# Optimization experiments

Hardware: AMD Instinct MI355X
Metric: run time of the kernel (lower is better)

Reference implementation:

```python
import jax, jax.numpy as jnp
import numpy as np

S, H, A = 8192, 4096, 1024

def setup_inputs() -> dict:
    key = jax.random.key(0)
    ks = jax.random.split(key, 8)
    return {
        "encoder_outputs": jax.random.normal(ks[0], (S, H), jnp.float32),
        "hidden": jax.random.normal(ks[1], (H,), jnp.float32),
        "U_w": jax.random.normal(ks[2], (A, H), jnp.float32) * (1.0 / np.sqrt(H)),
        "U_b": jax.random.normal(ks[3], (A,), jnp.float32) * 0.01,
        "W_w": jax.random.normal(ks[4], (A, H), jnp.float32) * (1.0 / np.sqrt(H)),
        "W_b": jax.random.normal(ks[5], (A,), jnp.float32) * 0.01,
        "V_w": jax.random.normal(ks[6], (1, A), jnp.float32) * (1.0 / np.sqrt(A)),
        "V_b": jax.random.normal(ks[7], (1,), jnp.float32) * 0.01,
    }

def reference(encoder_outputs, hidden, U_w, U_b, W_w, W_b, V_w, V_b):
    # Bahdanau additive attention ('add' mode).
    W_hidden = hidden @ W_w.T + W_b                      # [A]
    U_encode = encoder_outputs @ U_w.T + U_b             # [S, A]
    poly_tanh = jnp.tanh(U_encode + W_hidden)            # [S, A]
    scores = poly_tanh @ V_w.T + V_b                     # [S, 1]
    attn = jax.nn.softmax(scores, axis=0)                # softmax over sequence
    context = attn.T @ encoder_outputs                   # [1, H]
    return context[None]                                 # [1, 1, H] (matches torch bmm)
```

## Files before the change

### kernel.cpp

```cpp
#include <hip/hip_runtime.h>

typedef __attribute__((ext_vector_type(8))) short short8;
typedef __attribute__((ext_vector_type(4))) float f32x4;

#define S_DIM 8192
#define H_DIM 4096
#define A_DIM 1024

__device__ __forceinline__ short f2bf(float x) {
  unsigned u = __float_as_uint(x);
  u += 0x7fffu + ((u >> 16) & 1u);
  return (short)(u >> 16);
}

__device__ __forceinline__ float bf2f(short b) {
  return __uint_as_float(((unsigned)(unsigned short)b) << 16);
}

__device__ __forceinline__ void gload16(const void* g, void* l) {
  __builtin_amdgcn_global_load_lds(
      (const __attribute__((address_space(1))) void*)g,
      (__attribute__((address_space(3))) void*)l, 16, 0, 0);
}


__global__ __launch_bounds__(256) void comb_kernel(const float* __restrict__ hidden,
                                                   const float* __restrict__ Ww,
                                                   const float* __restrict__ Wb,
                                                   const float* __restrict__ Ub,
                                                   float* __restrict__ comb) {
  const int wave = threadIdx.x >> 6;
  const int lane = threadIdx.x & 63;
  const int a = blockIdx.x * 4 + wave;
  const float* row = Ww + (size_t)a * H_DIM;
  float acc = 0.f;
  for (int k = lane * 4; k < H_DIM; k += 64 * 4) {
    float4 w = *(const float4*)(row + k);
    float4 h = *(const float4*)(hidden + k);
    acc += w.x * h.x + w.y * h.y + w.z * h.z + w.w * h.w;
  }
  #pragma unroll
  for (int mk = 1; mk < 64; mk <<= 1) acc += __shfl_xor(acc, mk);
  if (lane == 0) comb[a] = acc + Wb[a] + Ub[a];
}

__global__ __launch_bounds__(1024) void softmax_kernel(const float* __restrict__ scores,
                                                       float* __restrict__ attn) {
  __shared__ float redm[16];
  __shared__ float reds[16];
  const int tid = threadIdx.x;
  const int lane = tid & 63, wid = tid >> 6;
  float v[8];
  float m = -3.0e38f;
  #pragma unroll
  for (int i = 0; i < 8; ++i) { v[i] = scores[i * 1024 + tid]; m = fmaxf(m, v[i]); }
  #pragma unroll
  for (int mk = 1; mk < 64; mk <<= 1) m = fmaxf(m, __shfl_xor(m, mk));
  if (lane == 0) redm[wid] = m;
  __syncthreads();
  float M = redm[0];
  #pragma unroll
  for (int j = 1; j < 16; ++j) M = fmaxf(M, redm[j]);
  float e[8]; float s = 0.f;
  #pragma unroll
  for (int i = 0; i < 8; ++i) { e[i] = __expf(v[i] - M); s += e[i]; }
  #pragma unroll
  for (int mk = 1; mk < 64; mk <<= 1) s += __shfl_xor(s, mk);
  if (lane == 0) reds[wid] = s;
  __syncthreads();
  float T = 0.f;
  #pragma unroll
  for (int j = 0; j < 16; ++j) T += reds[j];
  const float inv = 1.f / T;
  #pragma unroll
  for (int i = 0; i < 8; ++i) attn[i * 1024 + tid] = e[i] * inv;
}


__global__ __launch_bounds__(256) void cvt_kernel(const float* __restrict__ src,
                                                  unsigned short* __restrict__ dst,
                                                  int n8) {
  const int stride = gridDim.x * blockDim.x;
  for (int i = blockIdx.x * blockDim.x + threadIdx.x; i < n8; i += stride) {
    float4 a = ((const float4*)src)[(size_t)i * 2];
    float4 b = ((const float4*)src)[(size_t)i * 2 + 1];
    short8 o;
    o[0] = f2bf(a.x); o[1] = f2bf(a.y); o[2] = f2bf(a.z); o[3] = f2bf(a.w);
    o[4] = f2bf(b.x); o[5] = f2bf(b.y); o[6] = f2bf(b.z); o[7] = f2bf(b.w);
    ((short8*)dst)[i] = o;
  }
}

__global__ __launch_bounds__(256) void gemm_score_bf_kernel(
    const unsigned short* __restrict__ A,
    const unsigned short* __restrict__ B,
    const float* __restrict__ comb,
    const float* __restrict__ Vw,
    float* __restrict__ scores) {
  __shared__ __align__(16) unsigned short sA[128 * 64];
  __shared__ __align__(16) unsigned short sB[128 * 64];

  const int tid  = threadIdx.x;
  const int lane = tid & 63;
  const int wave = tid >> 6;
  const int wm = wave >> 1, wn = wave & 1;
  const int m0 = blockIdx.x * 128;
  const int n0 = blockIdx.y * 128;

  const int srow = wave * 32 + (lane >> 3);
  const int scol = (lane & 7) * 8;
  const unsigned short* ga = A + (size_t)(m0 + srow) * H_DIM + scol;
  const unsigned short* gb = B + (size_t)(n0 + srow) * H_DIM + scol;

  #define STAGE(kt) do {                                                     \
    const unsigned short* pa_ = ga + (size_t)(kt) * 64;                      \
    const unsigned short* pb_ = gb + (size_t)(kt) * 64;                      \
    _Pragma("unroll")                                                        \
    for (int i_ = 0; i_ < 4; ++i_) {                                         \
      gload16(pa_ + (size_t)i_ * 8 * H_DIM, &sA[(wave * 4 + i_) * 512]);     \
      gload16(pb_ + (size_t)i_ * 8 * H_DIM, &sB[(wave * 4 + i_) * 512]);     \
    }                                                                        \
  } while (0)

  f32x4 acc[4][4];
  const f32x4 zero = {0.f, 0.f, 0.f, 0.f};
  #pragma unroll
  for (int i = 0; i < 4; ++i)
    #pragma unroll
    for (int j = 0; j < 4; ++j) acc[i][j] = zero;

  STAGE(0);

  const int NK = H_DIM / 64;
  for (int kt = 0; kt < NK; ++kt) {
    __syncthreads();

    short8 af[2][4], bfr[2][4];
    #pragma unroll
    for (int ks = 0; ks < 2; ++ks) {
      #pragma unroll
      for (int i = 0; i < 4; ++i)
        af[ks][i] = *(const short8*)&sA[(wm * 64 + i * 16 + (lane & 15)) * 64 + ks * 32 + (lane >> 4) * 8];
      #pragma unroll
      for (int j = 0; j < 4; ++j)
        bfr[ks][j] = *(const short8*)&sB[(wn * 64 + j * 16 + (lane & 15)) * 64 + ks * 32 + (lane >> 4) * 8];
    }
    __syncthreads();

    if (kt + 1 < NK) STAGE(kt + 1);

    #pragma unroll
    for (int ks = 0; ks < 2; ++ks)
      #pragma unroll
      for (int i = 0; i < 4; ++i)
        #pragma unroll
        for (int j = 0; j < 4; ++j)
          acc[i][j] = __builtin_amdgcn_mfma_f32_16x16x32_bf16(af[ks][i], bfr[ks][j], acc[i][j], 0, 0, 0);
  }
  #undef STAGE

  float vwv[4], cbv[4];
  #pragma unroll
  for (int j = 0; j < 4; ++j) {
    const int col = n0 + wn * 64 + j * 16 + (lane & 15);
    vwv[j] = Vw[col];
    cbv[j] = comb[col];
  }
  #pragma unroll
  for (int i = 0; i < 4; ++i) {
    #pragma unroll
    for (int r = 0; r < 4; ++r) {
      float s = 0.f;
      #pragma unroll
      for (int j = 0; j < 4; ++j)
        s += vwv[j] * tanhf(acc[i][j][r] + cbv[j]);
      s += __shfl_xor(s, 1);
      s += __shfl_xor(s, 2);
      s += __shfl_xor(s, 4);
      s += __shfl_xor(s, 8);
      if ((lane & 15) == 0) {
        const int grow = m0 + wm * 64 + i * 16 + (lane >> 4) * 4 + r;
        atomicAdd(&scores[grow], s);
      }
    }
  }
}

__global__ __launch_bounds__(256) void context_bf_kernel(const unsigned short* __restrict__ Ebf,
                                                         const float* __restrict__ attn,
                                                         float* __restrict__ partial) {
  const int h0 = (blockIdx.x * 256 + threadIdx.x) * 8;
  const int s0 = blockIdx.y * 64;
  float acc[8] = {0.f, 0.f, 0.f, 0.f, 0.f, 0.f, 0.f, 0.f};
  for (int s = s0; s < s0 + 64; ++s) {
    const float w = attn[s];
    short8 e = *(const short8*)(Ebf + (size_t)s * H_DIM + h0);
    #pragma unroll
    for (int j = 0; j < 8; ++j) acc[j] += w * bf2f(e[j]);
  }
  float* p = partial + (size_t)blockIdx.y * H_DIM + h0;
  #pragma unroll
  for (int j = 0; j < 8; ++j) p[j] = acc[j];
}

__global__ __launch_bounds__(256) void context_reduce_kernel(const float* __restrict__ partial,
                                                             float* __restrict__ out) {
  const int h = blockIdx.x * 256 + threadIdx.x;
  float acc = 0.f;
  #pragma unroll 8
  for (int y = 0; y < 128; ++y) acc += partial[(size_t)y * H_DIM + h];
  out[h] = acc;
}


#define LDSW 40
__global__ __launch_bounds__(256) void gemm_score_kernel(const float* __restrict__ E,
                                                         const float* __restrict__ Uw,
                                                         const float* __restrict__ comb,
                                                         const float* __restrict__ Vw,
                                                         float* __restrict__ scores) {
  __shared__ __align__(16) short sA[128 * LDSW];
  __shared__ __align__(16) short sB[128 * LDSW];
  const int tid  = threadIdx.x;
  const int lane = tid & 63;
  const int wave = tid >> 6;
  const int wm = wave >> 1, wn = wave & 1;
  const int m0 = blockIdx.x * 128;
  const int n0 = blockIdx.y * 128;
  const int sr = tid >> 1;
  const int sh = tid & 1;
  const float* gA = E  + (size_t)(m0 + sr) * H_DIM + sh * 16;
  const float* gB = Uw + (size_t)(n0 + sr) * H_DIM + sh * 16;
  alignas(16) float fa[16], fb[16];
  #pragma unroll
  for (int j = 0; j < 4; ++j) {
    *(float4*)&fa[j * 4] = *(const float4*)(gA + j * 4);
    *(float4*)&fb[j * 4] = *(const float4*)(gB + j * 4);
  }
  f32x4 acc[4][4];
  const f32x4 zero = {0.f, 0.f, 0.f, 0.f};
  #pragma unroll
  for (int i = 0; i < 4; ++i)
    #pragma unroll
    for (int j = 0; j < 4; ++j) acc[i][j] = zero;
  short* wA = &sA[sr * LDSW + sh * 16];
  short* wB = &sB[sr * LDSW + sh * 16];
  const int NK = H_DIM / 32;
  for (int kt = 0; kt < NK; ++kt) {
    short8 ca0, ca1, cb0, cb1;
    #pragma unroll
    for (int j = 0; j < 8; ++j) {
      ca0[j] = f2bf(fa[j]);     ca1[j] = f2bf(fa[8 + j]);
      cb0[j] = f2bf(fb[j]);     cb1[j] = f2bf(fb[8 + j]);
    }
    __syncthreads();
    *(short8*)(wA)     = ca0;
    *(short8*)(wA + 8) = ca1;
    *(short8*)(wB)     = cb0;
    *(short8*)(wB + 8) = cb1;
    __syncthreads();
    if (kt + 1 < NK) {
      const float* pA = gA + (kt + 1) * 32;
      const float* pB = gB + (kt + 1) * 32;
      #pragma unroll
      for (int j = 0; j < 4; ++j) {
        *(float4*)&fa[j * 4] = *(const float4*)(pA + j * 4);
        *(float4*)&fb[j * 4] = *(const float4*)(pB + j * 4);
      }
    }
    short8 af[4], bfr[4];
    #pragma unroll
    for (int i = 0; i < 4; ++i)
      af[i] = *(const short8*)&sA[(wm * 64 + i * 16 + (lane & 15)) * LDSW + (lane >> 4) * 8];
    #pragma unroll
    for (int j = 0; j < 4; ++j)
      bfr[j] = *(const short8*)&sB[(wn * 64 + j * 16 + (lane & 15)) * LDSW + (lane >> 4) * 8];
    #pragma unroll
    for (int i = 0; i < 4; ++i)
      #pragma unroll
      for (int j = 0; j < 4; ++j)
        acc[i][j] = __builtin_amdgcn_mfma_f32_16x16x32_bf16(af[i], bfr[j], acc[i][j], 0, 0, 0);
  }
  float vwv[4], cbv[4];
  #pragma unroll
  for (int j = 0; j < 4; ++j) {
    const int col = n0 + wn * 64 + j * 16 + (lane & 15);
    vwv[j] = Vw[col];
    cbv[j] = comb[col];
  }
  #pragma unroll
  for (int i = 0; i < 4; ++i) {
    #pragma unroll
    for (int r = 0; r < 4; ++r) {
      float s = 0.f;
      #pragma unroll
      for (int j = 0; j < 4; ++j)
        s += vwv[j] * tanhf(acc[i][j][r] + cbv[j]);
      s += __shfl_xor(s, 1);
      s += __shfl_xor(s, 2);
      s += __shfl_xor(s, 4);
      s += __shfl_xor(s, 8);
      if ((lane & 15) == 0) {
        const int grow = m0 + wm * 64 + i * 16 + (lane >> 4) * 4 + r;
        atomicAdd(&scores[grow], s);
      }
    }
  }
}

__global__ __launch_bounds__(256) void context_kernel(const float* __restrict__ E,
                                                      const float* __restrict__ attn,
                                                      float* __restrict__ out) {
  const int h  = blockIdx.x * 256 + threadIdx.x;
  const int s0 = blockIdx.y * 256;
  float acc = 0.f;
  #pragma unroll 4
  for (int s = s0; s < s0 + 256; ++s)
    acc += attn[s] * E[(size_t)s * H_DIM + h];
  atomicAdd(&out[h], acc);
}


extern "C" void kernel_launch(void* const* d_in, const int* in_sizes, int n_in,
                              void* d_out, int out_size, void* d_ws, size_t ws_size,
                              hipStream_t stream) {
  const float* E   = (const float*)d_in[0];
  const float* hid = (const float*)d_in[1];
  const float* Uw  = (const float*)d_in[2];
  const float* Ub  = (const float*)d_in[3];
  const float* Ww  = (const float*)d_in[4];
  const float* Wb  = (const float*)d_in[5];
  const float* Vw  = (const float*)d_in[6];

  float* out    = (float*)d_out;
  float* ws     = (float*)d_ws;
  float* comb   = ws;
  float* scores = ws + 1024;
  float* attn   = ws + 1024 + 8192;

  float* partial = ws + 17408;
  unsigned short* Ebf  = (unsigned short*)(ws + 17408 + 128 * H_DIM);
  unsigned short* Uwbf = Ebf + (size_t)S_DIM * H_DIM;
  const size_t NEED = (size_t)(17408 + 128 * H_DIM) * 4
                    + (size_t)(S_DIM + A_DIM) * H_DIM * 2;

  hipMemsetAsync(scores, 0, S_DIM * sizeof(float), stream);

  comb_kernel<<<A_DIM / 4, 256, 0, stream>>>(hid, Ww, Wb, Ub, comb);

  if (ws_size >= NEED) {
    cvt_kernel<<<2048, 256, 0, stream>>>(E, Ebf, (int)((size_t)S_DIM * H_DIM / 8));
    cvt_kernel<<<512, 256, 0, stream>>>(Uw, Uwbf, (int)((size_t)A_DIM * H_DIM / 8));

    dim3 grid(S_DIM / 128, A_DIM / 128);
    gemm_score_bf_kernel<<<grid, 256, 0, stream>>>(Ebf, Uwbf, comb, Vw, scores);

    softmax_kernel<<<1, 1024, 0, stream>>>(scores, attn);

    context_bf_kernel<<<dim3(H_DIM / 2048, S_DIM / 64), 256, 0, stream>>>(Ebf, attn, partial);
    context_reduce_kernel<<<H_DIM / 256, 256, 0, stream>>>(partial, out);
  } else {
    hipMemsetAsync(out, 0, (size_t)out_size * sizeof(float), stream);
    dim3 grid(S_DIM / 128, A_DIM / 128);
    gemm_score_kernel<<<grid, 256, 0, stream>>>(E, Uw, comb, Vw, scores);
    softmax_kernel<<<1, 1024, 0, stream>>>(scores, attn);
    context_kernel<<<dim3(H_DIM / 256, 32), 256, 0, stream>>>(E, attn, out);
  }
}
```

Baseline: 156.7 us.

## Split score GEMM over K in two halves with separate tanh-score reduction kernel

The score GEMM gains a K dimension of 2 in its grid and now writes two fp32 partial [S,A] matrices to workspace instead of applying tanh and V in its epilogue. A new kernel sums the two partials, adds the bias, applies tanh, reduces against V per row, and writes scores directly, which also removes the scores memset and the atomics. The aim is to double the number of GEMM blocks (512 to 1024) to fill the CUs better. In exchange it writes and rereads about 64 MB of fp32 partials and adds a kernel launch. It also needs much more workspace, so if that is missing the code falls back to the old fused path.

After: 172.8 us. 10.3% more time.

```diff
diff --git a/kernel.cpp b/kernel.cpp
--- a/kernel.cpp
+++ b/kernel.cpp
@@ -22,7 +22,6 @@
       (const __attribute__((address_space(1))) void*)g,
       (__attribute__((address_space(3))) void*)l, 16, 0, 0);
 }
-
 
 __global__ __launch_bounds__(256) void comb_kernel(const float* __restrict__ hidden,
                                                    const float* __restrict__ Ww,
@@ -44,39 +43,6 @@
   if (lane == 0) comb[a] = acc + Wb[a] + Ub[a];
 }
 
-__global__ __launch_bounds__(1024) void softmax_kernel(const float* __restrict__ scores,
-                                                       float* __restrict__ attn) {
-  __shared__ float redm[16];
-  __shared__ float reds[16];
-  const int tid = threadIdx.x;
-  const int lane = tid & 63, wid = tid >> 6;
-  float v[8];
-  float m = -3.0e38f;
-  #pragma unroll
-  for (int i = 0; i < 8; ++i) { v[i] = scores[i * 1024 + tid]; m = fmaxf(m, v[i]); }
-  #pragma unroll
-  for (int mk = 1; mk < 64; mk <<= 1) m = fmaxf(m, __shfl_xor(m, mk));
-  if (lane == 0) redm[wid] = m;
-  __syncthreads();
-  float M = redm[0];
-  #pragma unroll
-  for (int j = 1; j < 16; ++j) M = fmaxf(M, redm[j]);
-  float e[8]; float s = 0.f;
-  #pragma unroll
-  for (int i = 0; i < 8; ++i) { e[i] = __expf(v[i] - M); s += e[i]; }
-  #pragma unroll
-  for (int mk = 1; mk < 64; mk <<= 1) s += __shfl_xor(s, mk);
-  if (lane == 0) reds[wid] = s;
-  __syncthreads();
-  float T = 0.f;
-  #pragma unroll
-  for (int j = 0; j < 16; ++j) T += reds[j];
-  const float inv = 1.f / T;
-  #pragma unroll
-  for (int i = 0; i < 8; ++i) attn[i * 1024 + tid] = e[i] * inv;
-}
-
-
 __global__ __launch_bounds__(256) void cvt_kernel(const float* __restrict__ src,
                                                   unsigned short* __restrict__ dst,
                                                   int n8) {
@@ -91,12 +57,10 @@
   }
 }
 
-__global__ __launch_bounds__(256) void gemm_score_bf_kernel(
+__global__ __launch_bounds__(256) void gemm_kspl_kernel(
     const unsigned short* __restrict__ A,
     const unsigned short* __restrict__ B,
-    const float* __restrict__ comb,
-    const float* __restrict__ Vw,
-    float* __restrict__ scores) {
+    float* __restrict__ partialC) {
   __shared__ __align__(16) unsigned short sA[128 * 64];
   __shared__ __align__(16) unsigned short sB[128 * 64];
 
@@ -106,11 +70,12 @@
   const int wm = wave >> 1, wn = wave & 1;
   const int m0 = blockIdx.x * 128;
   const int n0 = blockIdx.y * 128;
+  const int k0 = blockIdx.z * (H_DIM / 2);
 
   const int srow = wave * 32 + (lane >> 3);
   const int scol = (lane & 7) * 8;
-  const unsigned short* ga = A + (size_t)(m0 + srow) * H_DIM + scol;
-  const unsigned short* gb = B + (size_t)(n0 + srow) * H_DIM + scol;
+  const unsigned short* ga = A + (size_t)(m0 + srow) * H_DIM + k0 + scol;
+  const unsigned short* gb = B + (size_t)(n0 + srow) * H_DIM + k0 + scol;
 
   #define STAGE(kt) do {                                                     \
     const unsigned short* pa_ = ga + (size_t)(kt) * 64;                      \
@@ -131,10 +96,179 @@
 
   STAGE(0);
 
+  const int NK = (H_DIM / 2) / 64;
+  for (int kt = 0; kt < NK; ++kt) {
+    __syncthreads();
+
+    short8 af[2][4], bfr[2][4];
+    #pragma unroll
+    for (int ks = 0; ks < 2; ++ks) {
+      #pragma unroll
+      for (int i = 0; i < 4; ++i)
+        af[ks][i] = *(const short8*)&sA[(wm * 64 + i * 16 + (lane & 15)) * 64 + ks * 32 + (lane >> 4) * 8];
+      #pragma unroll
+      for (int j = 0; j < 4; ++j)
+        bfr[ks][j] = *(const short8*)&sB[(wn * 64 + j * 16 + (lane & 15)) * 64 + ks * 32 + (lane >> 4) * 8];
+    }
+    __syncthreads();
+
+    if (kt + 1 < NK) STAGE(kt + 1);
+
+    #pragma unroll
+    for (int ks = 0; ks < 2; ++ks)
+      #pragma unroll
+      for (int i = 0; i < 4; ++i)
+        #pragma unroll
+        for (int j = 0; j < 4; ++j)
+          acc[i][j] = __builtin_amdgcn_mfma_f32_16x16x32_bf16(af[ks][i], bfr[ks][j], acc[ks ? i : i][j], 0, 0, 0);
+  }
+  #undef STAGE
+
+  float* pc = partialC + (size_t)blockIdx.z * S_DIM * A_DIM;
+  #pragma unroll
+  for (int i = 0; i < 4; ++i) {
+    #pragma unroll
+    for (int r = 0; r < 4; ++r) {
+      const int grow = m0 + wm * 64 + i * 16 + (lane >> 4) * 4 + r;
+      float* prow = pc + (size_t)grow * A_DIM + n0 + wn * 64 + (lane & 15);
+      #pragma unroll
+      for (int j = 0; j < 4; ++j) prow[j * 16] = acc[i][j][r];
+    }
+  }
+}
+
+__global__ __launch_bounds__(256) void tanh_score_kernel(
+    const float* __restrict__ P,
+    const float* __restrict__ comb,
+    const float* __restrict__ Vw,
+    float* __restrict__ scores) {
+  const int lane = threadIdx.x & 63;
+  const int wave = threadIdx.x >> 6;
+  float4 vw[4], cb[4];
+  #pragma unroll
+  for (int c = 0; c < 4; ++c) {
+    vw[c] = *(const float4*)&Vw[c * 256 + lane * 4];
+    cb[c] = *(const float4*)&comb[c * 256 + lane * 4];
+  }
+  const float* P1 = P + (size_t)S_DIM * A_DIM;
+  const int row0 = (blockIdx.x * 4 + wave) * 4;
+  #pragma unroll
+  for (int rr = 0; rr < 4; ++rr) {
+    const int s = row0 + rr;
+    const float* p0 = P  + (size_t)s * A_DIM;
+    const float* p1 = P1 + (size_t)s * A_DIM;
+    float acc = 0.f;
+    #pragma unroll
+    for (int c = 0; c < 4; ++c) {
+      float4 x0 = *(const float4*)&p0[c * 256 + lane * 4];
+      float4 x1 = *(const float4*)&p1[c * 256 + lane * 4];
+      acc += vw[c].x * tanhf(x0.x + x1.x + cb[c].x);
+      acc += vw[c].y * tanhf(x0.y + x1.y + cb[c].y);
+      acc += vw[c].z * tanhf(x0.z + x1.z + cb[c].z);
+      acc += vw[c].w * tanhf(x0.w + x1.w + cb[c].w);
+    }
+    #pragma unroll
+    for (int mk = 1; mk < 64; mk <<= 1) acc += __shfl_xor(acc, mk);
+    if (lane == 0) scores[s] = acc;
+  }
+}
+
+__global__ __launch_bounds__(1024) void softmax_kernel(const float* __restrict__ scores,
+                                                       float* __restrict__ attn) {
+  __shared__ float redm[16];
+  __shared__ float reds[16];
+  const int tid = threadIdx.x;
+  const int lane = tid & 63, wid = tid >> 6;
+  float v[8];
+  float m = -3.0e38f;
+  #pragma unroll
+  for (int i = 0; i < 8; ++i) { v[i] = scores[i * 1024 + tid]; m = fmaxf(m, v[i]); }
+  #pragma unroll
+  for (int mk = 1; mk < 64; mk <<= 1) m = fmaxf(m, __shfl_xor(m, mk));
+  if (lane == 0) redm[wid] = m;
+  __syncthreads();
+  float M = redm[0];
+  #pragma unroll
+  for (int j = 1; j < 16; ++j) M = fmaxf(M, redm[j]);
+  float e[8]; float s = 0.f;
+  #pragma unroll
+  for (int i = 0; i < 8; ++i) { e[i] = __expf(v[i] - M); s += e[i]; }
+  #pragma unroll
+  for (int mk = 1; mk < 64; mk <<= 1) s += __shfl_xor(s, mk);
+  if (lane == 0) reds[wid] = s;
+  __syncthreads();
+  float T = 0.f;
+  #pragma unroll
+  for (int j = 0; j < 16; ++j) T += reds[j];
+  const float inv = 1.f / T;
+  #pragma unroll
+  for (int i = 0; i < 8; ++i) attn[i * 1024 + tid] = e[i] * inv;
+}
+
+__global__ __launch_bounds__(256) void context_bf_kernel(const unsigned short* __restrict__ Ebf,
+                                                         const float* __restrict__ attn,
+                                                         float* __restrict__ partial) {
+  const int h0 = (blockIdx.x * 256 + threadIdx.x) * 8;
+  const int s0 = blockIdx.y * 64;
+  float acc[8] = {0.f, 0.f, 0.f, 0.f, 0.f, 0.f, 0.f, 0.f};
+  for (int s = s0; s < s0 + 64; ++s) {
+    const float w = attn[s];
+    short8 e = *(const short8*)(Ebf + (size_t)s * H_DIM + h0);
+    #pragma unroll
+    for (int j = 0; j < 8; ++j) acc[j] += w * bf2f(e[j]);
+  }
+  float* p = partial + (size_t)blockIdx.y * H_DIM + h0;
+  #pragma unroll
+  for (int j = 0; j < 8; ++j) p[j] = acc[j];
+}
+
+__global__ __launch_bounds__(256) void context_reduce_kernel(const float* __restrict__ partial,
+                                                             float* __restrict__ out) {
+  const int h = blockIdx.x * 256 + threadIdx.x;
+  float acc = 0.f;
+  #pragma unroll 8
+  for (int y = 0; y < 128; ++y) acc += partial[(size_t)y * H_DIM + h];
+  out[h] = acc;
+}
+
+
+__global__ __launch_bounds__(256) void gemm_score_bf_kernel(
+    const unsigned short* __restrict__ A,
+    const unsigned short* __restrict__ B,
+    const float* __restrict__ comb,
+    const float* __restrict__ Vw,
+    float* __restrict__ scores) {
+  __shared__ __align__(16) unsigned short sA[128 * 64];
+  __shared__ __align__(16) unsigned short sB[128 * 64];
+  const int tid  = threadIdx.x;
+  const int lane = tid & 63;
+  const int wave = tid >> 6;
+  const int wm = wave >> 1, wn = wave & 1;
+  const int m0 = blockIdx.x * 128;
+  const int n0 = blockIdx.y * 128;
+  const int srow = wave * 32 + (lane >> 3);
+  const int scol = (lane & 7) * 8;
+  const unsigned short* ga = A + (size_t)(m0 + srow) * H_DIM + scol;
+  const unsigned short* gb = B + (size_t)(n0 + srow) * H_DIM + scol;
+  #define STAGE(kt) do {                                                     \
+    const unsigned short* pa_ = ga + (size_t)(kt) * 64;                      \
+    const unsigned short* pb_ = gb + (size_t)(kt) * 64;                      \
+    _Pragma("unroll")                                                        \
+    for (int i_ = 0; i_ < 4; ++i_) {                                         \
+      gload16(pa_ + (size_t)i_ * 8 * H_DIM, &sA[(wave * 4 + i_) * 512]);     \
+      gload16(pb_ + (size_t)i_ * 8 * H_DIM, &sB[(wave * 4 + i_) * 512]);     \
+    }                                                                        \
+  } while (0)
+  f32x4 acc[4][4];
+  const f32x4 zero = {0.f, 0.f, 0.f, 0.f};
+  #pragma unroll
+  for (int i = 0; i < 4; ++i)
+    #pragma unroll
+    for (int j = 0; j < 4; ++j) acc[i][j] = zero;
+  STAGE(0);
   const int NK = H_DIM / 64;
   for (int kt = 0; kt < NK; ++kt) {
     __syncthreads();
-
     short8 af[2][4], bfr[2][4];
     #pragma unroll
     for (int ks = 0; ks < 2; ++ks) {
@@ -146,9 +280,7 @@
         bfr[ks][j] = *(const short8*)&sB[(wn * 64 + j * 16 + (lane & 15)) * 64 + ks * 32 + (lane >> 4) * 8];
     }
     __syncthreads();
-
     if (kt + 1 < NK) STAGE(kt + 1);
-
     #pragma unroll
     for (int ks = 0; ks < 2; ++ks)
       #pragma unroll
@@ -158,7 +290,6 @@
           acc[i][j] = __builtin_amdgcn_mfma_f32_16x16x32_bf16(af[ks][i], bfr[ks][j], acc[i][j], 0, 0, 0);
   }
   #undef STAGE
-
   float vwv[4], cbv[4];
   #pragma unroll
   for (int j = 0; j < 4; ++j) {
@@ -186,140 +317,6 @@
   }
 }
 
-__global__ __launch_bounds__(256) void context_bf_kernel(const unsigned short* __restrict__ Ebf,
-                                                         const float* __restrict__ attn,
-                                                         float* __restrict__ partial) {
-  const int h0 = (blockIdx.x * 256 + threadIdx.x) * 8;
-  const int s0 = blockIdx.y * 64;
-  float acc[8] = {0.f, 0.f, 0.f, 0.f, 0.f, 0.f, 0.f, 0.f};
-  for (int s = s0; s < s0 + 64; ++s) {
-    const float w = attn[s];
-    short8 e = *(const short8*)(Ebf + (size_t)s * H_DIM + h0);
-    #pragma unroll
-    for (int j = 0; j < 8; ++j) acc[j] += w * bf2f(e[j]);
-  }
-  float* p = partial + (size_t)blockIdx.y * H_DIM + h0;
-  #pragma unroll
-  for (int j = 0; j < 8; ++j) p[j] = acc[j];
-}
-
-__global__ __launch_bounds__(256) void context_reduce_kernel(const float* __restrict__ partial,
-                                                             float* __restrict__ out) {
-  const int h = blockIdx.x * 256 + threadIdx.x;
-  float acc = 0.f;
-  #pragma unroll 8
-  for (int y = 0; y < 128; ++y) acc += partial[(size_t)y * H_DIM + h];
-  out[h] = acc;
-}
-
-
-#define LDSW 40
-__global__ __launch_bounds__(256) void gemm_score_kernel(const float* __restrict__ E,
-                                                         const float* __restrict__ Uw,
-                                                         const float* __restrict__ comb,
-                                                         const float* __restrict__ Vw,
-                                                         float* __restrict__ scores) {
-  __shared__ __align__(16) short sA[128 * LDSW];
-  __shared__ __align__(16) short sB[128 * LDSW];
-  const int tid  = threadIdx.x;
-  const int lane = tid & 63;
-  const int wave = tid >> 6;
-  const int wm = wave >> 1, wn = wave & 1;
-  const int m0 = blockIdx.x * 128;
-  const int n0 = blockIdx.y * 128;
-  const int sr = tid >> 1;
-  const int sh = tid & 1;
-  const float* gA = E  + (size_t)(m0 + sr) * H_DIM + sh * 16;
-  const float* gB = Uw + (size_t)(n0 + sr) * H_DIM + sh * 16;
-  alignas(16) float fa[16], fb[16];
-  #pragma unroll
-  for (int j = 0; j < 4; ++j) {
-    *(float4*)&fa[j * 4] = *(const float4*)(gA + j * 4);
-    *(float4*)&fb[j * 4] = *(const float4*)(gB + j * 4);
-  }
-  f32x4 acc[4][4];
-  const f32x4 zero = {0.f, 0.f, 0.f, 0.f};
-  #pragma unroll
-  for (int i = 0; i < 4; ++i)
-    #pragma unroll
-    for (int j = 0; j < 4; ++j) acc[i][j] = zero;
-  short* wA = &sA[sr * LDSW + sh * 16];
-  short* wB = &sB[sr * LDSW + sh * 16];
-  const int NK = H_DIM / 32;
-  for (int kt = 0; kt < NK; ++kt) {
-    short8 ca0, ca1, cb0, cb1;
-    #pragma unroll
-    for (int j = 0; j < 8; ++j) {
-      ca0[j] = f2bf(fa[j]);     ca1[j] = f2bf(fa[8 + j]);
-      cb0[j] = f2bf(fb[j]);     cb1[j] = f2bf(fb[8 + j]);
-    }
-    __syncthreads();
-    *(short8*)(wA)     = ca0;
-    *(short8*)(wA + 8) = ca1;
-    *(short8*)(wB)     = cb0;
-    *(short8*)(wB + 8) = cb1;
-    __syncthreads();
-    if (kt + 1 < NK) {
-      const float* pA = gA + (kt + 1) * 32;
-      const float* pB = gB + (kt + 1) * 32;
-      #pragma unroll
-      for (int j = 0; j < 4; ++j) {
-        *(float4*)&fa[j * 4] = *(const float4*)(pA + j * 4);
-        *(float4*)&fb[j * 4] = *(const float4*)(pB + j * 4);
-      }
-    }
-    short8 af[4], bfr[4];
-    #pragma unroll
-    for (int i = 0; i < 4; ++i)
-      af[i] = *(const short8*)&sA[(wm * 64 + i * 16 + (lane & 15)) * LDSW + (lane >> 4) * 8];
-    #pragma unroll
-    for (int j = 0; j < 4; ++j)
-      bfr[j] = *(const short8*)&sB[(wn * 64 + j * 16 + (lane & 15)) * LDSW + (lane >> 4) * 8];
-    #pragma unroll
-    for (int i = 0; i < 4; ++i)
-      #pragma unroll
-      for (int j = 0; j < 4; ++j)
-        acc[i][j] = __builtin_amdgcn_mfma_f32_16x16x32_bf16(af[i], bfr[j], acc[i][j], 0, 0, 0);
-  }
-  float vwv[4], cbv[4];
-  #pragma unroll
-  for (int j = 0; j < 4; ++j) {
-    const int col = n0 + wn * 64 + j * 16 + (lane & 15);
-    vwv[j] = Vw[col];
-    cbv[j] = comb[col];
-  }
-  #pragma unroll
-  for (int i = 0; i < 4; ++i) {
-    #pragma unroll
-    for (int r = 0; r < 4; ++r) {
-      float s = 0.f;
-      #pragma unroll
-      for (int j = 0; j < 4; ++j)
-        s += vwv[j] * tanhf(acc[i][j][r] + cbv[j]);
-      s += __shfl_xor(s, 1);
-      s += __shfl_xor(s, 2);
-      s += __shfl_xor(s, 4);
-      s += __shfl_xor(s, 8);
-      if ((lane & 15) == 0) {
-        const int grow = m0 + wm * 64 + i * 16 + (lane >> 4) * 4 + r;
-        atomicAdd(&scores[grow], s);
-      }
-    }
-  }
-}
-
-__global__ __launch_bounds__(256) void context_kernel(const float* __restrict__ E,
-                                                      const float* __restrict__ attn,
-                                                      float* __restrict__ out) {
-  const int h  = blockIdx.x * 256 + threadIdx.x;
-  const int s0 = blockIdx.y * 256;
-  float acc = 0.f;
-  #pragma unroll 4
-  for (int s = s0; s < s0 + 256; ++s)
-    acc += attn[s] * E[(size_t)s * H_DIM + h];
-  atomicAdd(&out[h], acc);
-}
-
 
 extern "C" void kernel_launch(void* const* d_in, const int* in_sizes, int n_in,
                               void* d_out, int out_size, void* d_ws, size_t ws_size,
@@ -337,33 +334,41 @@
   float* comb   = ws;
   float* scores = ws + 1024;
   float* attn   = ws + 1024 + 8192;
-
-  float* partial = ws + 17408;
-  unsigned short* Ebf  = (unsigned short*)(ws + 17408 + 128 * H_DIM);
-  unsigned short* Uwbf = Ebf + (size_t)S_DIM * H_DIM;
-  const size_t NEED = (size_t)(17408 + 128 * H_DIM) * 4
-                    + (size_t)(S_DIM + A_DIM) * H_DIM * 2;
-
-  hipMemsetAsync(scores, 0, S_DIM * sizeof(float), stream);
+  float* ctxp   = ws + 17408;
+  const size_t CTXP = (size_t)128 * H_DIM;
+
+  float* pC = ws + 17408 + CTXP;
+  unsigned short* Ebf2  = (unsigned short*)(pC + 2 * (size_t)S_DIM * A_DIM);
+  unsigned short* Uwbf2 = Ebf2 + (size_t)S_DIM * H_DIM;
+  const size_t NEED2 = ((size_t)17408 + CTXP + 2 * (size_t)S_DIM * A_DIM) * 4
+                     + ((size_t)S_DIM + A_DIM) * H_DIM * 2;
+
+  unsigned short* Ebf1  = (unsigned short*)(ws + 17408 + CTXP);
+  unsigned short* Uwbf1 = Ebf1 + (size_t)S_DIM * H_DIM;
+  const size_t NEED1 = ((size_t)17408 + CTXP) * 4
+                     + ((size_t)S_DIM + A_DIM) * H_DIM * 2;
 
   comb_kernel<<<A_DIM / 4, 256, 0, stream>>>(hid, Ww, Wb, Ub, comb);
 
-  if (ws_size >= NEED) {
-    cvt_kernel<<<2048, 256, 0, stream>>>(E, Ebf, (int)((size_t)S_DIM * H_DIM / 8));
-    cvt_kernel<<<512, 256, 0, stream>>>(Uw, Uwbf, (int)((size_t)A_DIM * H_DIM / 8));
-
-    dim3 grid(S_DIM / 128, A_DIM / 128);
-    gemm_score_bf_kernel<<<grid, 256, 0, stream>>>(Ebf, Uwbf, comb, Vw, scores);
+  if (ws_size >= NEED2) {
+    cvt_kernel<<<2048, 256, 0, stream>>>(E, Ebf2, (int)((size_t)S_DIM * H_DIM / 8));
+    cvt_kernel<<<512, 256, 0, stream>>>(Uw, Uwbf2, (int)((size_t)A_DIM * H_DIM / 8));
+
+    gemm_kspl_kernel<<<dim3(S_DIM / 128, A_DIM / 128, 2), 256, 0, stream>>>(Ebf2, Uwbf2, pC);
+    tanh_score_kernel<<<512, 256, 0, stream>>>(pC, comb, Vw, scores);
 
     softmax_kernel<<<1, 1024, 0, stream>>>(scores, attn);
 
-    context_bf_kernel<<<dim3(H_DIM / 2048, S_DIM / 64), 256, 0, stream>>>(Ebf, attn, partial);
-    context_reduce_kernel<<<H_DIM / 256, 256, 0, stream>>>(partial, out);
+    context_bf_kernel<<<dim3(H_DIM / 2048, S_DIM / 64), 256, 0, stream>>>(Ebf2, attn, ctxp);
+    context_reduce_kernel<<<H_DIM / 256, 256, 0, stream>>>(ctxp, out);
   } else {
-    hipMemsetAsync(out, 0, (size_t)out_size * sizeof(float), stream);
-    dim3 grid(S_DIM / 128, A_DIM / 128);
-    gemm_score_kernel<<<grid, 256, 0, stream>>>(E, Uw, comb, Vw, scores);
+    hipMemsetAsync(scores, 0, S_DIM * sizeof(float), stream);
+    cvt_kernel<<<2048, 256, 0, stream>>>(E, Ebf1, (int)((size_t)S_DIM * H_DIM / 8));
+    cvt_kernel<<<512, 256, 0, stream>>>(Uw, Uwbf1, (int)((size_t)A_DIM * H_DIM / 8));
+
+    gemm_score_bf_kernel<<<dim3(S_DIM / 128, A_DIM / 128), 256, 0, stream>>>(Ebf1, Uwbf1, comb, Vw, scores);
     softmax_kernel<<<1, 1024, 0, stream>>>(scores, attn);
-    context_kernel<<<dim3(H_DIM / 256, 32), 256, 0, stream>>>(E, attn, out);
-  }
-}
+    context_bf_kernel<<<dim3(H_DIM / 2048, S_DIM / 64), 256, 0, stream>>>(Ebf1, attn, ctxp);
+    context_reduce_kernel<<<H_DIM / 256, 256, 0, stream>>>(ctxp, out);
+  }
+}
```
